# Kernel tuning notes

Measured on AMD Instinct MI355X. Metric: run time of the kernel, lower is better.

## Reference

```python
import jax, jax.numpy as jnp
import numpy as np

N = 50000          # nodes
E = 800000         # edges
D_IN = 64          # env INPUT_DIM
D_H = 64           # env HIDDEN_DIM
D_OUT = 32         # env OUTPUT_DIM
A_H = 16           # action HIDDEN_DIM
NUM_ENV = 3        # env NUM_LAYERS
TAU = 1.0          # gumbel temperature (fixed, LEARN_TEMPERATURE=False)
LN_EPS = 1e-5


def setup_inputs() -> dict:
    key = jax.random.key(0)
    ks = jax.random.split(key, 24)

    def lin(k, fan_in, fan_out):
        s = 1.0 / np.sqrt(fan_in)
        kw, kb = jax.random.split(k)
        W = jax.random.uniform(kw, (fan_in, fan_out), jnp.float32, -s, s)
        b = jax.random.uniform(kb, (fan_out,), jnp.float32, -s, s)
        return W, b

    inp = {}
    inp['x'] = jax.random.normal(ks[0], (N, D_IN), jnp.float32)
    inp['edge_index'] = jax.random.randint(ks[1], (2, E), 0, N, dtype=jnp.int32)

    inp['W_enc'], inp['b_enc'] = lin(ks[2], D_IN, D_H)
    env_W, env_b = [], []
    for l in range(NUM_ENV):
        W, b = lin(ks[3 + l], 2 * D_H, D_H)
        env_W.append(W); env_b.append(b)
    inp['env_W'] = jnp.stack(env_W)   # [NUM_ENV, 2*D_H, D_H]
    inp['env_b'] = jnp.stack(env_b)   # [NUM_ENV, D_H]
    inp['W_dec'], inp['b_dec'] = lin(ks[6], D_H, D_OUT)
    inp['ln_g'] = jnp.ones((D_H,), jnp.float32)
    inp['ln_b'] = jnp.zeros((D_H,), jnp.float32)
    inp['in_W1'], inp['in_b1'] = lin(ks[7], 2 * D_H, A_H)
    inp['in_W2'], inp['in_b2'] = lin(ks[8], 2 * A_H, 2)
    inp['out_W1'], inp['out_b1'] = lin(ks[9], 2 * D_H, A_H)
    inp['out_W2'], inp['out_b2'] = lin(ks[10], 2 * A_H, 2)
    return inp


def _layernorm(x, g, b):
    mu = jnp.mean(x, axis=-1, keepdims=True)
    var = jnp.var(x, axis=-1, keepdims=True)
    return (x - mu) * jax.lax.rsqrt(var + LN_EPS) * g + b


def _conv(x, src, dst, W, b, edge_weight=None):
    # WeightedGNNConv: gather x[src] -> (optional * edge_weight) -> scatter-add at dst -> lin(concat(x, agg))
    msg = x[src]                                   # [E, d]
    if edge_weight is not None:
        msg = msg * edge_weight[:, None]
    agg = jax.ops.segment_sum(msg, dst, num_segments=N)
    return jnp.concatenate([x, agg], axis=-1) @ W + b


def _action_net(x, src, dst, W1, b1, W2, b2):
    h = jax.nn.relu(_conv(x, src, dst, W1, b1))
    return _conv(h, src, dst, W2, b2)              # [N, 2] logits


def _gumbel_hard(logits, key, tau):
    u = jax.random.uniform(key, logits.shape, logits.dtype, 1e-20, 1.0)
    g = -jnp.log(-jnp.log(u))
    y = jax.nn.softmax((logits + g) / tau, axis=-1)
    y_hard = jax.nn.one_hot(jnp.argmax(y, axis=-1), logits.shape[-1], dtype=y.dtype)
    return y + jax.lax.stop_gradient(y_hard - y)   # straight-through


def reference(x, edge_index, W_enc, b_enc, env_W, env_b, W_dec, b_dec, ln_g, ln_b,
              in_W1, in_b1, in_W2, in_b2, out_W1, out_b1, out_W2, out_b2):
    src, dst = edge_index[0], edge_index[1]        # u, v
    h = x @ W_enc + b_enc                          # encoder (dropout is identity in eval)
    noise_key = jax.random.key(1234)
    ews = []
    for l in range(NUM_ENV):
        h = _layernorm(h, ln_g, ln_b)
        in_logits = _action_net(h, src, dst, in_W1, in_b1, in_W2, in_b2)
        out_logits = _action_net(h, src, dst, out_W1, out_b1, out_W2, out_b2)
        in_p = _gumbel_hard(in_logits, jax.random.fold_in(noise_key, 2 * l), TAU)
        out_p = _gumbel_hard(out_logits, jax.random.fold_in(noise_key, 2 * l + 1), TAU)
        # create_edge_weight: keep_in_prob[v] * keep_out_prob[u]
        ew = in_p[:, 0][dst] * out_p[:, 0][src]    # [E], values in {0,1}
        ews.append(ew)
        h = _conv(h, src, dst, env_W[l], env_b[l], edge_weight=ew)
    out = h @ W_dec + b_dec
    return out, jnp.stack(ews)
```

## Files before the change

### kernel.cpp

```cpp
#include <hip/hip_runtime.h>
#include <math.h>

static constexpr int NN = 50000;
static constexpr int EE = 800000;

typedef unsigned long long ull;

struct TF2 { unsigned a, b; };

__host__ __device__ __forceinline__ TF2 tf2x32(unsigned k0, unsigned k1,
                                               unsigned x0, unsigned x1) {
  unsigned k2 = k0 ^ k1 ^ 0x1BD11BDAu;
  x0 += k0; x1 += k1;
#define TFR(r) { x0 += x1; x1 = (x1 << (r)) | (x1 >> (32 - (r))); x1 ^= x0; }
  TFR(13) TFR(15) TFR(26) TFR(6)
  x0 += k1; x1 += k2 + 1u;
  TFR(17) TFR(29) TFR(16) TFR(24)
  x0 += k2; x1 += k0 + 2u;
  TFR(13) TFR(15) TFR(26) TFR(6)
  x0 += k0; x1 += k1 + 3u;
  TFR(17) TFR(29) TFR(16) TFR(24)
  x0 += k1; x1 += k2 + 4u;
  TFR(13) TFR(15) TFR(26) TFR(6)
  x0 += k2; x1 += k0 + 5u;
#undef TFR
  TF2 r; r.a = x0; r.b = x1; return r;
}

__device__ __forceinline__ float u01_bits(unsigned w) {
  float fl = __uint_as_float((w >> 9) | 0x3f800000u) - 1.0f;
  return fmaxf(1e-20f, fl + 1e-20f);
}

__device__ __forceinline__ float keep01(float l0, float l1, unsigned k0, unsigned k1, int node) {
  unsigned f0 = 2u * (unsigned)node, f1 = f0 + 1u;
  TF2 t0 = tf2x32(k0, k1, 0u, f0);
  TF2 t1 = tf2x32(k0, k1, 0u, f1);
  float g0 = -logf(-logf(u01_bits(t0.a ^ t0.b)));
  float g1 = -logf(-logf(u01_bits(t1.a ^ t1.b)));
  float z0 = l0 + g0, z1 = l1 + g1;
  float m  = fmaxf(z0, z1);
  float e0 = expf(z0 - m), e1 = expf(z1 - m);
  float s  = e0 + e1;
  float y0 = e0 / s, y1 = e1 / s;
  return (y1 > y0) ? 0.0f : 1.0f;
}

__global__ void k_count(const int* __restrict__ dst, int* __restrict__ deg, int e) {
  int i = blockIdx.x * blockDim.x + threadIdx.x;
  if (i < e) atomicAdd(&deg[dst[i]], 1);
}

__global__ void k_bsum(const int* __restrict__ deg, int* __restrict__ bsum, int n) {
  int i = blockIdx.x * 256 + threadIdx.x;
  int v = (i < n) ? deg[i] : 0;
  #pragma unroll
  for (int off = 32; off; off >>= 1) v += __shfl_xor(v, off, 64);
  __shared__ int ws[4];
  if ((threadIdx.x & 63) == 0) ws[threadIdx.x >> 6] = v;
  __syncthreads();
  if (threadIdx.x == 0) bsum[blockIdx.x] = ws[0] + ws[1] + ws[2] + ws[3];
}

__global__ void k_bscan(const int* __restrict__ bsum, int* __restrict__ bpref,
                        int nb, int* __restrict__ row_ptr, int n) {
  __shared__ int s[256];
  int t = threadIdx.x;
  int v = (t < nb) ? bsum[t] : 0;
  s[t] = v; __syncthreads();
  for (int off = 1; off < 256; off <<= 1) {
    int u = (t >= off) ? s[t - off] : 0;
    __syncthreads();
    s[t] += u;
    __syncthreads();
  }
  bpref[t] = s[t] - v;
  if (t == 0) row_ptr[n] = s[255];
}

__global__ void k_prefix(const int* __restrict__ deg, const int* __restrict__ bpref,
                         int* __restrict__ row_ptr, int* __restrict__ cursor, int n) {
  __shared__ int s[256];
  int t = threadIdx.x;
  int i = blockIdx.x * 256 + t;
  int v = (i < n) ? deg[i] : 0;
  s[t] = v; __syncthreads();
  for (int off = 1; off < 256; off <<= 1) {
    int u = (t >= off) ? s[t - off] : 0;
    __syncthreads();
    s[t] += u;
    __syncthreads();
  }
  if (i < n) {
    int ex = s[t] - v + bpref[blockIdx.x];
    row_ptr[i] = ex; cursor[i] = ex;
  }
}

__global__ void k_fill(const int* __restrict__ src, const int* __restrict__ dst,
                       int* __restrict__ cursor, ull* __restrict__ ce, int e) {
  int i = blockIdx.x * blockDim.x + threadIdx.x;
  if (i < e) {
    int pos = atomicAdd(&cursor[dst[i]], 1);
    ce[pos] = ((ull)(unsigned)src[i] << 20) | (unsigned)i;
  }
}

__global__ void k_enc_ln(const float* __restrict__ x, const float* __restrict__ W,
                         const float* __restrict__ bias, const float* __restrict__ g,
                         const float* __restrict__ bb, float* __restrict__ hln) {
  __shared__ float Ws[64 * 64];
  for (int i = threadIdx.x; i < 64 * 64; i += 256) Ws[i] = W[i];
  __syncthreads();
  int node = blockIdx.x * 4 + (threadIdx.x >> 6);
  int j = threadIdx.x & 63;
  const float* xr = x + (size_t)node * 64;
  float s = bias[j];
  #pragma unroll
  for (int i = 0; i < 64; i++) s = fmaf(xr[i], Ws[i * 64 + j], s);
  float t = s;
  #pragma unroll
  for (int off = 32; off; off >>= 1) t += __shfl_xor(t, off, 64);
  float mu = t * (1.0f / 64.0f);
  float d = s - mu;
  float q = d * d;
  #pragma unroll
  for (int off = 32; off; off >>= 1) q += __shfl_xor(q, off, 64);
  float rs = 1.0f / sqrtf(q * (1.0f / 64.0f) + 1e-5f);
  hln[(size_t)node * 64 + j] = d * rs * g[j] + bb[j];
}

__global__ void k_proj(const float* __restrict__ hln,
                       const float* __restrict__ W1i, const float* __restrict__ W1o,
                       float* __restrict__ P1, float* __restrict__ S1, int nchunk) {
  int t = threadIdx.x, w = t >> 6, lane = t & 63;
  int h = lane >> 5, jo = lane & 31;
  const float* Wg = (jo < 16) ? W1i : W1o;
  int col = jo & 15;
  float wr[64];
  #pragma unroll
  for (int i = 0; i < 64; i++) wr[i] = Wg[(h * 64 + i) * 16 + col];
  __shared__ float st[256];
  for (int blk = blockIdx.x; blk < nchunk; blk += gridDim.x) {
    __syncthreads();
    st[t] = hln[(size_t)blk * 256 + t];
    __syncthreads();
    const float* sv = &st[w * 64];
    float a = 0.f;
    #pragma unroll
    for (int i = 0; i < 64; i++) a = fmaf(sv[i], wr[i], a);
    size_t node = (size_t)blk * 4 + w;
    if (h == 0) S1[node * 32 + jo] = a;
    else        P1[node * 32 + jo] = a;
  }
}

__global__ void k_projE(const float* __restrict__ hln, const float* __restrict__ W,
                        const float* __restrict__ bias,
                        float* __restrict__ Htop, float* __restrict__ Pbot, int nchunk) {
  __shared__ float Ws[128 * 64];
  __shared__ float st[256];
  int t = threadIdx.x;
  for (int i = t; i < 128 * 64; i += 256) Ws[i] = W[i];
  int w = t >> 6, lane = t & 63;
  float bj = bias[lane];
  for (int blk = blockIdx.x; blk < nchunk; blk += gridDim.x) {
    __syncthreads();
    st[t] = hln[(size_t)blk * 256 + t];
    __syncthreads();
    const float* sv = &st[w * 64];
    float a = bj, b = 0.f;
    #pragma unroll
    for (int i = 0; i < 64; i++) {
      float hv = sv[i];
      a = fmaf(hv, Ws[i * 64 + lane], a);
      b = fmaf(hv, Ws[(64 + i) * 64 + lane], b);
    }
    size_t node = (size_t)blk * 4 + w;
    Htop[node * 64 + lane] = a;
    Pbot[node * 64 + lane] = b;
  }
}

__global__ void k_gatherA(const float* __restrict__ P1, const float* __restrict__ S1,
                          const int* __restrict__ row_ptr, const ull* __restrict__ ce,
                          const float* __restrict__ inb1, const float* __restrict__ outb1,
                          const float* __restrict__ inW2, const float* __restrict__ outW2,
                          float* __restrict__ P2S2) {
  int t = threadIdx.x;
  int w = t >> 6, lane = t & 63;
  int sub = lane >> 5, j = lane & 31;
  int node = blockIdx.x * 8 + w * 2 + sub;
  int b = row_ptr[node], e = row_ptr[node + 1];
  float s0 = 0.f, s1 = 0.f;
  for (int base = b; base < e; base += 32) {
    int idx = base + j;
    int u_l = (idx < e) ? (int)(ce[idx] >> 20) : 0;
    int cnt = min(32, e - base);
    int k = 0;
    for (; k + 2 <= cnt; k += 2) {
      int u0 = __shfl(u_l, k, 32), u1 = __shfl(u_l, k + 1, 32);
      s0 += P1[(size_t)u0 * 32 + j];
      s1 += P1[(size_t)u1 * 32 + j];
    }
    if (k < cnt) s0 += P1[(size_t)__shfl(u_l, k, 32) * 32 + j];
  }
  float agg = s0 + s1;
  float b1j = (j < 16) ? inb1[j] : outb1[j - 16];
  float rj = fmaxf(S1[(size_t)node * 32 + j] + agg + b1j, 0.f);
  float wa0, wa1, wb0, wb1;
  if (j < 16) {
    wa0 = inW2[j * 2 + 0];  wa1 = inW2[j * 2 + 1];
    wb0 = inW2[(16 + j) * 2 + 0];  wb1 = inW2[(16 + j) * 2 + 1];
  } else {
    int j2 = j - 16;
    wa0 = outW2[j2 * 2 + 0];  wa1 = outW2[j2 * 2 + 1];
    wb0 = outW2[(16 + j2) * 2 + 0];  wb1 = outW2[(16 + j2) * 2 + 1];
  }
  float v0 = rj * wa0, v1 = rj * wa1, v2 = rj * wb0, v3 = rj * wb1;
  #pragma unroll
  for (int off = 8; off; off >>= 1) {
    v0 += __shfl_xor(v0, off, 64);
    v1 += __shfl_xor(v1, off, 64);
    v2 += __shfl_xor(v2, off, 64);
    v3 += __shfl_xor(v3, off, 64);
  }
  float* row = P2S2 + (size_t)node * 8;
  if (j == 0)  { row[0] = v2; row[1] = v3; row[4] = v0; row[5] = v1; }
  if (j == 16) { row[2] = v2; row[3] = v3; row[6] = v0; row[7] = v1; }
}

__global__ void k_gatherB(const float* __restrict__ P2S2, const int* __restrict__ row_ptr,
                          const ull* __restrict__ ce,
                          const float* __restrict__ inb2, const float* __restrict__ outb2,
                          float* __restrict__ keep_in, float* __restrict__ keep_out,
                          unsigned ki0, unsigned ki1, unsigned ko0, unsigned ko1) {
  int t = threadIdx.x;
  int w = t >> 6, lane = t & 63;
  int g = lane >> 4, el = lane & 15;
  int node = blockIdx.x * 16 + w * 4 + g;
  int b = row_ptr[node], e = row_ptr[node + 1];
  float a0 = 0.f, a1 = 0.f, a2 = 0.f, a3 = 0.f;
  for (int base = b; base < e; base += 16) {
    int idx = base + el;
    if (idx < e) {
      int u = (int)(ce[idx] >> 20);
      float4 p = *(const float4*)(P2S2 + (size_t)u * 8);
      a0 += p.x; a1 += p.y; a2 += p.z; a3 += p.w;
    }
  }
  #pragma unroll
  for (int off = 8; off; off >>= 1) {
    a0 += __shfl_xor(a0, off, 64);
    a1 += __shfl_xor(a1, off, 64);
    a2 += __shfl_xor(a2, off, 64);
    a3 += __shfl_xor(a3, off, 64);
  }
  float4 sf = *(const float4*)(P2S2 + (size_t)node * 8 + 4);
  if (el == 0)
    keep_in[node]  = keep01(sf.x + a0 + inb2[0],  sf.y + a1 + inb2[1],  ki0, ki1, node);
  else if (el == 1)
    keep_out[node] = keep01(sf.z + a2 + outb2[0], sf.w + a3 + outb2[1], ko0, ko1, node);
}

template <bool LN>
__global__ void k_aggD(const float* __restrict__ Htop, const float* __restrict__ Pbot,
                       const int* __restrict__ row_ptr, const ull* __restrict__ ce,
                       const float* __restrict__ keep_in, const float* __restrict__ keep_out,
                       float* __restrict__ ew, const float* __restrict__ g,
                       const float* __restrict__ bb, float* __restrict__ hout) {
  int t = threadIdx.x;
  int w = t >> 6, lane = t & 63;
  int node = blockIdx.x * 4 + w;
  float ki = keep_in[node];
  int b = row_ptr[node], e = row_ptr[node + 1];
  float s0 = 0.f, s1 = 0.f, s2 = 0.f, s3 = 0.f;
  for (int base = b; base < e; base += 64) {
    int idx = base + lane;
    int u_l = 0; float ko_l = 0.f;
    if (idx < e) {
      ull c = ce[idx];
      u_l = (int)(c >> 20);
      ko_l = keep_out[u_l];
      ew[(unsigned)(c & 0xFFFFFu)] = ki * ko_l;
    }
    if (ki != 0.f) {
      int cnt = min(64, e - base);
      int k = 0;
      for (; k + 4 <= cnt; k += 4) {
        int u0 = __shfl(u_l, k, 64),     u1 = __shfl(u_l, k + 1, 64),
            u2 = __shfl(u_l, k + 2, 64), u3 = __shfl(u_l, k + 3, 64);
        float w0 = __shfl(ko_l, k, 64),     w1 = __shfl(ko_l, k + 1, 64),
              w2 = __shfl(ko_l, k + 2, 64), w3 = __shfl(ko_l, k + 3, 64);
        if (w0 != 0.f) s0 += Pbot[(size_t)u0 * 64 + lane];
        if (w1 != 0.f) s1 += Pbot[(size_t)u1 * 64 + lane];
        if (w2 != 0.f) s2 += Pbot[(size_t)u2 * 64 + lane];
        if (w3 != 0.f) s3 += Pbot[(size_t)u3 * 64 + lane];
      }
      for (; k < cnt; k++) {
        int u0 = __shfl(u_l, k, 64);
        float w0 = __shfl(ko_l, k, 64);
        if (w0 != 0.f) s0 += Pbot[(size_t)u0 * 64 + lane];
      }
    }
  }
  float acc = Htop[(size_t)node * 64 + lane] + ((s0 + s1) + (s2 + s3)) * ki;
  if (LN) {
    float tt = acc;
    #pragma unroll
    for (int off = 32; off; off >>= 1) tt += __shfl_xor(tt, off, 64);
    float mu = tt * (1.0f / 64.0f);
    float d = acc - mu;
    float q = d * d;
    #pragma unroll
    for (int off = 32; off; off >>= 1) q += __shfl_xor(q, off, 64);
    float rs = 1.0f / sqrtf(q * (1.0f / 64.0f) + 1e-5f);
    hout[(size_t)node * 64 + lane] = d * rs * g[lane] + bb[lane];
  } else {
    hout[(size_t)node * 64 + lane] = acc;
  }
}

__global__ void k_dec(const float* __restrict__ h, const float* __restrict__ W,
                      const float* __restrict__ bias, float* __restrict__ out) {
  __shared__ float Ws[64 * 32];
  int t = threadIdx.x;
  for (int i = t; i < 64 * 32; i += 256) Ws[i] = W[i];
  __syncthreads();
  int node = blockIdx.x * 8 + (t >> 5);
  int j = t & 31;
  const float* hr = h + (size_t)node * 64;
  float s = bias[j];
  #pragma unroll
  for (int i = 0; i < 64; i++) s = fmaf(hr[i], Ws[i * 32 + j], s);
  out[(size_t)node * 32 + j] = s;
}

extern "C" void kernel_launch(void* const* d_in, const int* in_sizes, int n_in,
                              void* d_out, int out_size, void* d_ws, size_t ws_size,
                              hipStream_t stream) {
  const float* x      = (const float*)d_in[0];
  const int*   ei     = (const int*)  d_in[1];
  const float* W_enc  = (const float*)d_in[2];
  const float* b_enc  = (const float*)d_in[3];
  const float* env_W  = (const float*)d_in[4];
  const float* env_b  = (const float*)d_in[5];
  const float* W_dec  = (const float*)d_in[6];
  const float* b_dec  = (const float*)d_in[7];
  const float* ln_g   = (const float*)d_in[8];
  const float* ln_b   = (const float*)d_in[9];
  const float* in_W1  = (const float*)d_in[10];
  const float* in_b1  = (const float*)d_in[11];
  const float* in_W2  = (const float*)d_in[12];
  const float* in_b2  = (const float*)d_in[13];
  const float* out_W1 = (const float*)d_in[14];
  const float* out_b1 = (const float*)d_in[15];
  const float* out_W2 = (const float*)d_in[16];
  const float* out_b2 = (const float*)d_in[17];

  const int n = NN, e = EE;
  const int* src = ei;
  const int* dst = ei + e;

  float* out_h  = (float*)d_out;
  float* out_ew = out_h + (size_t)n * 32;

  size_t off = 0;
  auto alloc = [&](size_t bytes) -> void* {
    void* p = (char*)d_ws + off;
    off += (bytes + 255) & ~(size_t)255;
    return p;
  };
  float* hlnA    = (float*)alloc((size_t)n * 64 * 4);
  float* hlnB    = (float*)alloc((size_t)n * 64 * 4);
  float* Htop    = (float*)alloc((size_t)n * 64 * 4);
  float* Pbot    = (float*)alloc((size_t)n * 64 * 4);
  float* P1      = (float*)alloc((size_t)n * 32 * 4);
  float* S1      = (float*)alloc((size_t)n * 32 * 4);
  float* P2S2    = (float*)alloc((size_t)n * 8 * 4);
  float* keep_i  = (float*)alloc((size_t)n * 4);
  float* keep_o  = (float*)alloc((size_t)n * 4);
  int*   deg     = (int*)alloc((size_t)n * 4);
  int*   row_ptr = (int*)alloc((size_t)(n + 1) * 4);
  int*   cursor  = (int*)alloc((size_t)n * 4);
  int*   bsum    = (int*)alloc(256 * 4);
  int*   bpref   = (int*)alloc(256 * 4);
  ull*   ce      = (ull*)alloc((size_t)e * 8);
  if (off > ws_size) return;

  const int nb = (n + 255) / 256;

  hipMemsetAsync(deg, 0, (size_t)n * 4, stream);
  k_count<<<(e + 255) / 256, 256, 0, stream>>>(dst, deg, e);
  k_bsum<<<nb, 256, 0, stream>>>(deg, bsum, n);
  k_bscan<<<1, 256, 0, stream>>>(bsum, bpref, nb, row_ptr, n);
  k_prefix<<<nb, 256, 0, stream>>>(deg, bpref, row_ptr, cursor, n);
  k_fill<<<(e + 255) / 256, 256, 0, stream>>>(src, dst, cursor, ce, e);

  const int g4  = n / 4;
  const int g8  = n / 8;
  const int g16 = n / 16;

  k_enc_ln<<<g4, 256, 0, stream>>>(x, W_enc, b_enc, ln_g, ln_b, hlnA);

  float* hln = hlnA;
  float* hln_next = hlnB;
  for (int l = 0; l < 3; l++) {
    TF2 kin  = tf2x32(0u, 1234u, 0u, (unsigned)(2 * l));
    TF2 kout = tf2x32(0u, 1234u, 0u, (unsigned)(2 * l + 1));

    k_projE<<<1250, 256, 0, stream>>>(hln, env_W + (size_t)l * 128 * 64,
                                      env_b + (size_t)l * 64, Htop, Pbot, g4);
    k_proj<<<1250, 256, 0, stream>>>(hln, in_W1, out_W1, P1, S1, g4);
    k_gatherA<<<g8, 256, 0, stream>>>(P1, S1, row_ptr, ce, in_b1, out_b1,
                                      in_W2, out_W2, P2S2);
    k_gatherB<<<g16, 256, 0, stream>>>(P2S2, row_ptr, ce, in_b2, out_b2,
                                       keep_i, keep_o, kin.a, kin.b, kout.a, kout.b);
    if (l < 2) {
      k_aggD<true><<<g4, 256, 0, stream>>>(Htop, Pbot, row_ptr, ce, keep_i, keep_o,
                                           out_ew + (size_t)l * e, ln_g, ln_b, hln_next);
    } else {
      k_aggD<false><<<g4, 256, 0, stream>>>(Htop, Pbot, row_ptr, ce, keep_i, keep_o,
                                            out_ew + (size_t)l * e, ln_g, ln_b, hln_next);
    }
    float* tmp = hln; hln = hln_next; hln_next = tmp;
  }

  k_dec<<<g8, 256, 0, stream>>>(hln, W_dec, b_dec, out_h);
}
```

Baseline: 643.0 us.

## Shrink CSR entries to int, fuse projections, write edge weights in original order

The CSR edge array changes from 64-bit packed (src, edge id) to 32-bit src only, which halves index traffic in every gather kernel. Edge weights are now written coalesced in original edge order: the first 64 threads of each aggD block compute keep_in[dst]*keep_out[src], replacing the scattered writes through the stored edge id. The env and action-net first-layer projections are fused into one kernel so hln is read once per layer. The cost is extra random reads of keep_in and keep_out, plus the fused kernel's register and LDS footprint.

```diff
diff --git a/kernel.cpp b/kernel.cpp
--- a/kernel.cpp
+++ b/kernel.cpp
@@ -3,8 +3,6 @@
 
 static constexpr int NN = 50000;
 static constexpr int EE = 800000;
-
-typedef unsigned long long ull;
 
 struct TF2 { unsigned a, b; };
 
@@ -98,11 +96,11 @@
 }
 
 __global__ void k_fill(const int* __restrict__ src, const int* __restrict__ dst,
-                       int* __restrict__ cursor, ull* __restrict__ ce, int e) {
+                       int* __restrict__ cursor, int* __restrict__ col, int e) {
   int i = blockIdx.x * blockDim.x + threadIdx.x;
   if (i < e) {
     int pos = atomicAdd(&cursor[dst[i]], 1);
-    ce[pos] = ((ull)(unsigned)src[i] << 20) | (unsigned)i;
+    col[pos] = src[i];
   }
 }
 
@@ -130,60 +128,46 @@
   hln[(size_t)node * 64 + j] = d * rs * g[j] + bb[j];
 }
 
-__global__ void k_proj(const float* __restrict__ hln,
-                       const float* __restrict__ W1i, const float* __restrict__ W1o,
-                       float* __restrict__ P1, float* __restrict__ S1, int nchunk) {
-  int t = threadIdx.x, w = t >> 6, lane = t & 63;
+__global__ void k_projAll(const float* __restrict__ hln, const float* __restrict__ envW,
+                          const float* __restrict__ envb,
+                          const float* __restrict__ W1i, const float* __restrict__ W1o,
+                          float* __restrict__ Htop, float* __restrict__ Pbot,
+                          float* __restrict__ P1, float* __restrict__ S1, int nchunk) {
+  __shared__ float Ws[128 * 64];
+  __shared__ float st[256];
+  int t = threadIdx.x;
+  for (int i = t; i < 128 * 64; i += 256) Ws[i] = envW[i];
+  int w = t >> 6, lane = t & 63;
   int h = lane >> 5, jo = lane & 31;
   const float* Wg = (jo < 16) ? W1i : W1o;
-  int col = jo & 15;
+  int colw = jo & 15;
   float wr[64];
   #pragma unroll
-  for (int i = 0; i < 64; i++) wr[i] = Wg[(h * 64 + i) * 16 + col];
-  __shared__ float st[256];
+  for (int i = 0; i < 64; i++) wr[i] = Wg[(h * 64 + i) * 16 + colw];
+  float bj = envb[lane];
   for (int blk = blockIdx.x; blk < nchunk; blk += gridDim.x) {
     __syncthreads();
     st[t] = hln[(size_t)blk * 256 + t];
     __syncthreads();
     const float* sv = &st[w * 64];
-    float a = 0.f;
-    #pragma unroll
-    for (int i = 0; i < 64; i++) a = fmaf(sv[i], wr[i], a);
-    size_t node = (size_t)blk * 4 + w;
-    if (h == 0) S1[node * 32 + jo] = a;
-    else        P1[node * 32 + jo] = a;
-  }
-}
-
-__global__ void k_projE(const float* __restrict__ hln, const float* __restrict__ W,
-                        const float* __restrict__ bias,
-                        float* __restrict__ Htop, float* __restrict__ Pbot, int nchunk) {
-  __shared__ float Ws[128 * 64];
-  __shared__ float st[256];
-  int t = threadIdx.x;
-  for (int i = t; i < 128 * 64; i += 256) Ws[i] = W[i];
-  int w = t >> 6, lane = t & 63;
-  float bj = bias[lane];
-  for (int blk = blockIdx.x; blk < nchunk; blk += gridDim.x) {
-    __syncthreads();
-    st[t] = hln[(size_t)blk * 256 + t];
-    __syncthreads();
-    const float* sv = &st[w * 64];
-    float a = bj, b = 0.f;
+    float a = bj, b = 0.f, c = 0.f;
     #pragma unroll
     for (int i = 0; i < 64; i++) {
       float hv = sv[i];
       a = fmaf(hv, Ws[i * 64 + lane], a);
       b = fmaf(hv, Ws[(64 + i) * 64 + lane], b);
+      c = fmaf(hv, wr[i], c);
     }
     size_t node = (size_t)blk * 4 + w;
     Htop[node * 64 + lane] = a;
     Pbot[node * 64 + lane] = b;
+    if (h == 0) S1[node * 32 + jo] = c;
+    else        P1[node * 32 + jo] = c;
   }
 }
 
 __global__ void k_gatherA(const float* __restrict__ P1, const float* __restrict__ S1,
-                          const int* __restrict__ row_ptr, const ull* __restrict__ ce,
+                          const int* __restrict__ row_ptr, const int* __restrict__ col,
                           const float* __restrict__ inb1, const float* __restrict__ outb1,
                           const float* __restrict__ inW2, const float* __restrict__ outW2,
                           float* __restrict__ P2S2) {
@@ -195,7 +179,7 @@
   float s0 = 0.f, s1 = 0.f;
   for (int base = b; base < e; base += 32) {
     int idx = base + j;
-    int u_l = (idx < e) ? (int)(ce[idx] >> 20) : 0;
+    int u_l = (idx < e) ? col[idx] : 0;
     int cnt = min(32, e - base);
     int k = 0;
     for (; k + 2 <= cnt; k += 2) {
@@ -231,7 +215,7 @@
 }
 
 __global__ void k_gatherB(const float* __restrict__ P2S2, const int* __restrict__ row_ptr,
-                          const ull* __restrict__ ce,
+                          const int* __restrict__ col,
                           const float* __restrict__ inb2, const float* __restrict__ outb2,
                           float* __restrict__ keep_in, float* __restrict__ keep_out,
                           unsigned ki0, unsigned ki1, unsigned ko0, unsigned ko1) {
@@ -244,7 +228,7 @@
   for (int base = b; base < e; base += 16) {
     int idx = base + el;
     if (idx < e) {
-      int u = (int)(ce[idx] >> 20);
+      int u = col[idx];
       float4 p = *(const float4*)(P2S2 + (size_t)u * 8);
       a0 += p.x; a1 += p.y; a2 += p.z; a3 += p.w;
     }
@@ -265,26 +249,26 @@
 
 template <bool LN>
 __global__ void k_aggD(const float* __restrict__ Htop, const float* __restrict__ Pbot,
-                       const int* __restrict__ row_ptr, const ull* __restrict__ ce,
+                       const int* __restrict__ row_ptr, const int* __restrict__ col,
+                       const int* __restrict__ src, const int* __restrict__ dst,
                        const float* __restrict__ keep_in, const float* __restrict__ keep_out,
                        float* __restrict__ ew, const float* __restrict__ g,
                        const float* __restrict__ bb, float* __restrict__ hout) {
   int t = threadIdx.x;
+  int ei = blockIdx.x * 64 + t;
+  if (t < 64 && ei < EE)
+    ew[ei] = keep_in[dst[ei]] * keep_out[src[ei]];
+
   int w = t >> 6, lane = t & 63;
   int node = blockIdx.x * 4 + w;
   float ki = keep_in[node];
   int b = row_ptr[node], e = row_ptr[node + 1];
   float s0 = 0.f, s1 = 0.f, s2 = 0.f, s3 = 0.f;
-  for (int base = b; base < e; base += 64) {
-    int idx = base + lane;
-    int u_l = 0; float ko_l = 0.f;
-    if (idx < e) {
-      ull c = ce[idx];
-      u_l = (int)(c >> 20);
-      ko_l = keep_out[u_l];
-      ew[(unsigned)(c & 0xFFFFFu)] = ki * ko_l;
-    }
-    if (ki != 0.f) {
+  if (ki != 0.f) {
+    for (int base = b; base < e; base += 64) {
+      int idx = base + lane;
+      int u_l = (idx < e) ? col[idx] : 0;
+      float ko_l = (idx < e) ? keep_out[u_l] : 0.f;
       int cnt = min(64, e - base);
       int k = 0;
       for (; k + 4 <= cnt; k += 4) {
@@ -385,7 +369,7 @@
   int*   cursor  = (int*)alloc((size_t)n * 4);
   int*   bsum    = (int*)alloc(256 * 4);
   int*   bpref   = (int*)alloc(256 * 4);
-  ull*   ce      = (ull*)alloc((size_t)e * 8);
+  int*   colA    = (int*)alloc((size_t)e * 4);
   if (off > ws_size) return;
 
   const int nb = (n + 255) / 256;
@@ -395,7 +379,7 @@
   k_bsum<<<nb, 256, 0, stream>>>(deg, bsum, n);
   k_bscan<<<1, 256, 0, stream>>>(bsum, bpref, nb, row_ptr, n);
   k_prefix<<<nb, 256, 0, stream>>>(deg, bpref, row_ptr, cursor, n);
-  k_fill<<<(e + 255) / 256, 256, 0, stream>>>(src, dst, cursor, ce, e);
+  k_fill<<<(e + 255) / 256, 256, 0, stream>>>(src, dst, cursor, colA, e);
 
   const int g4  = n / 4;
   const int g8  = n / 8;
@@ -409,19 +393,21 @@
     TF2 kin  = tf2x32(0u, 1234u, 0u, (unsigned)(2 * l));
     TF2 kout = tf2x32(0u, 1234u, 0u, (unsigned)(2 * l + 1));
 
-    k_projE<<<1250, 256, 0, stream>>>(hln, env_W + (size_t)l * 128 * 64,
-                                      env_b + (size_t)l * 64, Htop, Pbot, g4);
-    k_proj<<<1250, 256, 0, stream>>>(hln, in_W1, out_W1, P1, S1, g4);
-    k_gatherA<<<g8, 256, 0, stream>>>(P1, S1, row_ptr, ce, in_b1, out_b1,
+    k_projAll<<<1250, 256, 0, stream>>>(hln, env_W + (size_t)l * 128 * 64,
+                                        env_b + (size_t)l * 64, in_W1, out_W1,
+                                        Htop, Pbot, P1, S1, g4);
+    k_gatherA<<<g8, 256, 0, stream>>>(P1, S1, row_ptr, colA, in_b1, out_b1,
                                       in_W2, out_W2, P2S2);
-    k_gatherB<<<g16, 256, 0, stream>>>(P2S2, row_ptr, ce, in_b2, out_b2,
+    k_gatherB<<<g16, 256, 0, stream>>>(P2S2, row_ptr, colA, in_b2, out_b2,
                                        keep_i, keep_o, kin.a, kin.b, kout.a, kout.b);
     if (l < 2) {
-      k_aggD<true><<<g4, 256, 0, stream>>>(Htop, Pbot, row_ptr, ce, keep_i, keep_o,
-                                           out_ew + (size_t)l * e, ln_g, ln_b, hln_next);
+      k_aggD<true><<<g4, 256, 0, stream>>>(Htop, Pbot, row_ptr, colA, src, dst,
+                                           keep_i, keep_o, out_ew + (size_t)l * e,
+                                           ln_g, ln_b, hln_next);
     } else {
-      k_aggD<false><<<g4, 256, 0, stream>>>(Htop, Pbot, row_ptr, ce, keep_i, keep_o,
-                                            out_ew + (size_t)l * e, ln_g, ln_b, hln_next);
+      k_aggD<false><<<g4, 256, 0, stream>>>(Htop, Pbot, row_ptr, colA, src, dst,
+                                            keep_i, keep_o, out_ew + (size_t)l * e,
+                                            ln_g, ln_b, hln_next);
     }
     float* tmp = hln; hln = hln_next; hln_next = tmp;
   }
```

After: 656.8 us. 1.02x slower.
